# Optimization experiments

Measured on AMD Instinct MI355X. Metric: run time of the kernel, lower is better.

Reference implementation:

```python
import jax, jax.numpy as jnp
import numpy as np
from jax import lax

DN = ('NHWC', 'HWIO', 'NHWC')


def setup_inputs() -> dict:
    key = jax.random.key(0)
    k1, k2, k3, k4, k5, k6 = jax.random.split(key, 6)
    B = 1024
    vals = jax.random.normal(k1, (B, 64, 64, 1), dtype=jnp.float32)
    active = (jax.random.uniform(k2, (B, 64, 64, 1)) < 0.1).astype(jnp.float32)
    x = vals * active
    W1 = jax.random.normal(k3, (3, 3, 1, 64), dtype=jnp.float32) * 0.1
    b1 = jax.random.normal(k4, (64,), dtype=jnp.float32) * 0.1
    W2 = jax.random.normal(k5, (3, 3, 64, 32), dtype=jnp.float32) * 0.05
    b2 = jax.random.normal(k6, (32,), dtype=jnp.float32) * 0.05
    return {"x": x, "W1": W1, "b1": b1, "W2": W2, "b2": b2}


def reference(x, W1, b1, W2, b2):
    # x: [B, 64, 64, 1] NHWC (spconv from_dense layout); active sites = nonzero pixels
    m0 = (jnp.abs(x).max(axis=-1, keepdims=True) > 0).astype(x.dtype)  # [B,64,64,1]
    # SparseConv2d(1,64,3,stride=1, pad=0): output indices = any active input in 3x3 window
    m1 = lax.reduce_window(m0, jnp.array(0, x.dtype), lax.max,
                           (1, 3, 3, 1), (1, 1, 1, 1), 'VALID')  # [B,62,62,1]
    y = lax.conv_general_dilated(x, W1, (1, 1), 'VALID', dimension_numbers=DN)
    y = (y + b1) * m1  # bias only at active output sites; [B,62,62,64]
    # SparseInverseConv2d(64,32,3): transposed conv restricted to the ORIGINAL
    # active index set (indice_key='cp0'), i.e. output only where m0 is active.
    z = lax.conv_transpose(y, W2, (1, 1), 'VALID', dimension_numbers=DN)  # [B,64,64,32]
    z = (z + b2) * m0
    # SparseConvTensor.dense() returns NCHW
    return jnp.transpose(z, (0, 3, 1, 2))
```

## Files before the change

### kernel.cpp

```cpp
#include <hip/hip_runtime.h>

#define BDIM 256
#define KC_STRIDE 28
#define CASE_STRIDE (32 * KC_STRIDE)
#define SP 2052

typedef float floatx4 __attribute__((ext_vector_type(4)));

__device__ __forceinline__ int casef(int p) {
  return ((unsigned)(p - 2) < 60u) ? 2 : (p < 2 ? p : p - 59);
}

__global__ __launch_bounds__(BDIM) void prep_kernel(
    const float* __restrict__ W1, const float* __restrict__ b1,
    const float* __restrict__ W2, const float* __restrict__ b2,
    float* __restrict__ ws) {
  __shared__ float Mlds[9 * 9 * 32];
  __shared__ float BvL[9 * 32];
  const int tid = threadIdx.x;
  const int co = tid & 31;
  for (int tap = tid >> 5; tap < 9; tap += 8) {
    float acc[9] = {0.f, 0.f, 0.f, 0.f, 0.f, 0.f, 0.f, 0.f, 0.f};
    float accB = 0.f;
    for (int ci = 0; ci < 64; ++ci) {
      float w2 = W2[(tap * 64 + ci) * 32 + co];
      accB = fmaf(b1[ci], w2, accB);
#pragma unroll
      for (int e = 0; e < 9; ++e) acc[e] = fmaf(W1[e * 64 + ci], w2, acc[e]);
    }
#pragma unroll
    for (int e = 0; e < 9; ++e) Mlds[(tap * 9 + e) * 32 + co] = acc[e];
    BvL[tap * 32 + co] = accB;
  }
  __syncthreads();

  const int a = blockIdx.x / 5, c = blockIdx.x % 5;
  const int dmask[5] = {4, 6, 7, 3, 1};
  const int Da = dmask[a], Dc = dmask[c];
  for (int t = tid; t < CASE_STRIDE; t += BDIM) {
    int cc = t / KC_STRIDE, r = t % KC_STRIDE;
    float s = 0.f;
    if (r < 25) {
      int u = r / 5, v = r % 5;
      for (int di = 0; di < 3; ++di) {
        if (!((Da >> di) & 1)) continue;
        int ei = u - di;
        if ((unsigned)ei > 2u) continue;
        for (int dj = 0; dj < 3; ++dj) {
          if (!((Dc >> dj) & 1)) continue;
          int ej = v - dj;
          if ((unsigned)ej > 2u) continue;
          s += Mlds[((di * 3 + dj) * 9 + ei * 3 + ej) * 32 + cc];
        }
      }
    } else if (r == 25) {
      s = b2[cc];
      for (int di = 0; di < 3; ++di)
        if ((Da >> di) & 1)
          for (int dj = 0; dj < 3; ++dj)
            if ((Dc >> dj) & 1) s += BvL[(di * 3 + dj) * 32 + cc];
    }
    ws[blockIdx.x * CASE_STRIDE + t] = s;
  }
}

__global__ __launch_bounds__(BDIM) void main_kernel(
    const float* __restrict__ x, const float* __restrict__ ws,
    float* __restrict__ out) {
  const int bb = blockIdx.x;
  const int b = bb >> 1;
  const int r0 = (bb & 1) << 5;
  const int tid = threadIdx.x;
  const int lane = tid & 63;
  const int wave = tid >> 6;

  __shared__ __align__(16) float xp[36 * 68];
  __shared__ __align__(16) float S[8][SP];
  __shared__ __align__(16) float KiL[CASE_STRIDE];
  __shared__ unsigned long long Rm[32];
  __shared__ unsigned short aqi[448], aqb[128];
  __shared__ int nqi_sh, nqb_sh;

  if (tid == 0) { nqi_sh = 0; nqb_sh = 0; }
  float4* xp4 = reinterpret_cast<float4*>(xp);
  for (int i = tid; i < 612; i += BDIM) xp4[i] = make_float4(0.f, 0.f, 0.f, 0.f);
  for (int i = tid; i < CASE_STRIDE; i += BDIM) KiL[i] = ws[12 * CASE_STRIDE + i];
  __syncthreads();

  const float* xb = x + (size_t)b * 4096;
  for (int it = tid; it < 576; it += BDIM) {
    int i = it >> 4, c4 = (it & 15) << 2;
    int r = r0 - 2 + i;
    if ((unsigned)r < 64u) {
      float4 v = *reinterpret_cast<const float4*>(xb + r * 64 + c4);
      float2* d2 = reinterpret_cast<float2*>(&xp[i * 68 + 2 + c4]);
      d2[0] = make_float2(v.x, v.y);
      d2[1] = make_float2(v.z, v.w);
    }
  }
  __syncthreads();

  for (int k = wave; k < 32; k += 4) {
    int pred = (xp[(k + 2) * 68 + 2 + lane] != 0.0f);
    unsigned long long m = __ballot(pred);
    if (lane == 0) Rm[k] = m;
  }
  __syncthreads();

  for (int g = tid; g < 512; g += BDIM) {
    int k = g >> 4, q0 = (g & 15) << 2;
    unsigned bits = (unsigned)(Rm[k] >> q0) & 0xFu;
    if (!bits) continue;
    int p = r0 + k;
    bool inter = ((unsigned)(p - 2) < 60u) && ((unsigned)(q0 - 4) <= 52u);
    if (inter) {
      aqi[atomicAdd(&nqi_sh, 1)] = (unsigned short)g;
    } else {
      aqb[atomicAdd(&nqb_sh, 1)] = (unsigned short)g;
    }
  }
  __syncthreads();

  const int nqi = nqi_sh, nqb = nqb_sh;
  float* outb = out + (size_t)b * (32 * 4096);
  const int co4 = tid & 3;

  for (int cg = 0; cg < 4; ++cg) {
    const int co_lo = (cg << 3) + co4;
    float KA[26], KB[26];
    {
      const float* KpA = &KiL[co_lo * KC_STRIDE];
      const float* KpB = &KiL[(co_lo + 4) * KC_STRIDE];
#pragma unroll
      for (int j = 0; j < 26; ++j) { KA[j] = KpA[j]; KB[j] = KpB[j]; }
    }
    for (int n = tid; n < nqi * 4; n += BDIM) {
      int g = aqi[n >> 2];
      int k = g >> 4, q0 = (g & 15) << 2;
      float ba = KA[25], bbv = KB[25];
      float a0 = ba, a1 = ba, a2 = ba, a3 = ba;
      float b0 = bbv, b1 = bbv, b2 = bbv, b3 = bbv;
#pragma unroll
      for (int u = 0; u < 5; ++u) {
        const float* xr = &xp[(k + u) * 68 + q0];
        float4 xa = *reinterpret_cast<const float4*>(xr);
        float4 xc = *reinterpret_cast<const float4*>(xr + 4);
        float xv[8] = {xa.x, xa.y, xa.z, xa.w, xc.x, xc.y, xc.z, xc.w};
#pragma unroll
        for (int v = 0; v < 5; ++v) {
          float ka = KA[u * 5 + v], kb = KB[u * 5 + v];
          a0 = fmaf(xv[v], ka, a0);
          a1 = fmaf(xv[v + 1], ka, a1);
          a2 = fmaf(xv[v + 2], ka, a2);
          a3 = fmaf(xv[v + 3], ka, a3);
          b0 = fmaf(xv[v], kb, b0);
          b1 = fmaf(xv[v + 1], kb, b1);
          b2 = fmaf(xv[v + 2], kb, b2);
          b3 = fmaf(xv[v + 3], kb, b3);
        }
      }
      int so = (k << 6) + q0;
      *reinterpret_cast<float4*>(&S[co4][so]) = make_float4(a0, a1, a2, a3);
      *reinterpret_cast<float4*>(&S[co4 + 4][so]) = make_float4(b0, b1, b2, b3);
    }
    for (int n = tid; n < nqb * 8; n += BDIM) {
      int g = aqb[n >> 3];
      int cs = n & 7;
      int co = (cg << 3) + cs;
      int k = g >> 4, q0 = (g & 15) << 2;
      int p = r0 + k;
      int cp = casef(p);
      const float* K0 = ws + ((cp * 5 + casef(q0)) * 32 + co) * KC_STRIDE;
      const float* K1 = ws + ((cp * 5 + casef(q0 + 1)) * 32 + co) * KC_STRIDE;
      const float* K2 = ws + ((cp * 5 + casef(q0 + 2)) * 32 + co) * KC_STRIDE;
      const float* K3 = ws + ((cp * 5 + casef(q0 + 3)) * 32 + co) * KC_STRIDE;
      float z0 = K0[25], z1 = K1[25], z2 = K2[25], z3 = K3[25];
#pragma unroll
      for (int u = 0; u < 5; ++u) {
        const float* xr = &xp[(k + u) * 68 + q0];
        float4 xa = *reinterpret_cast<const float4*>(xr);
        float4 xc = *reinterpret_cast<const float4*>(xr + 4);
        float xv[8] = {xa.x, xa.y, xa.z, xa.w, xc.x, xc.y, xc.z, xc.w};
#pragma unroll
        for (int v = 0; v < 5; ++v) {
          int o = u * 5 + v;
          z0 = fmaf(xv[v], K0[o], z0);
          z1 = fmaf(xv[v + 1], K1[o], z1);
          z2 = fmaf(xv[v + 2], K2[o], z2);
          z3 = fmaf(xv[v + 3], K3[o], z3);
        }
      }
      *reinterpret_cast<float4*>(&S[cs][(k << 6) + q0]) =
          make_float4(z0, z1, z2, z3);
    }
    asm volatile("s_waitcnt lgkmcnt(0)" ::: "memory");
    __builtin_amdgcn_s_barrier();
    {
      int co_a = (cg << 3) + wave;
      float* dstA = outb + (((size_t)co_a) << 12) + (r0 << 6);
      float* dstB = outb + (((size_t)(co_a + 4)) << 12) + (r0 << 6);
      const floatx4* SpA = reinterpret_cast<const floatx4*>(&S[wave][0]);
      const floatx4* SpB = reinterpret_cast<const floatx4*>(&S[wave + 4][0]);
#pragma unroll
      for (int i = 0; i < 8; ++i) {
        int f4 = (i << 6) + lane;
        int kk = f4 >> 4, q0 = (f4 & 15) << 2;
        unsigned bits = (unsigned)(Rm[kk] >> q0) & 0xFu;
        floatx4 va = SpA[f4];
        floatx4 vb = SpB[f4];
        if (!(bits & 1u)) { va.x = 0.f; vb.x = 0.f; }
        if (!(bits & 2u)) { va.y = 0.f; vb.y = 0.f; }
        if (!(bits & 4u)) { va.z = 0.f; vb.z = 0.f; }
        if (!(bits & 8u)) { va.w = 0.f; vb.w = 0.f; }
        __builtin_nontemporal_store(va, reinterpret_cast<floatx4*>(dstA + (f4 << 2)));
        __builtin_nontemporal_store(vb, reinterpret_cast<floatx4*>(dstB + (f4 << 2)));
      }
    }
    asm volatile("s_waitcnt lgkmcnt(0)" ::: "memory");
    __builtin_amdgcn_s_barrier();
  }
}

extern "C" void kernel_launch(void* const* d_in, const int* in_sizes, int n_in,
                              void* d_out, int out_size, void* d_ws, size_t ws_size,
                              hipStream_t stream) {
  const float* x  = (const float*)d_in[0];
  const float* W1 = (const float*)d_in[1];
  const float* b1 = (const float*)d_in[2];
  const float* W2 = (const float*)d_in[3];
  const float* b2 = (const float*)d_in[4];
  float* out = (float*)d_out;
  float* ws  = (float*)d_ws;
  int B = in_sizes[0] / 4096;

  hipLaunchKernelGGL(prep_kernel, dim3(25), dim3(BDIM), 0, stream, W1, b1, W2, b2, ws);
  hipLaunchKernelGGL(main_kernel, dim3(2 * B), dim3(BDIM), 0, stream, x, ws, out);
}
```

Baseline: 123.8 us.

## Process whole 64-row image per block instead of half-image blocks

Each block now handles a full 64x64 image instead of a 32-row half, halving the grid to B blocks and removing the two-row halo reloaded by each half. Shared buffers (padded input, staging S, active-group queues) are doubled. This cuts redundant halo loads and per-block setup such as the weight copy into LDS, at the cost of much larger LDS use per block, which lowers occupancy, and fewer blocks to spread across CUs.

```diff
diff --git a/kernel.cpp b/kernel.cpp
--- a/kernel.cpp
+++ b/kernel.cpp
@@ -3,7 +3,7 @@
 #define BDIM 256
 #define KC_STRIDE 28
 #define CASE_STRIDE (32 * KC_STRIDE)
-#define SP 2052
+#define SP 4100
 
 typedef float floatx4 __attribute__((ext_vector_type(4)));
 
@@ -67,51 +67,45 @@
 __global__ __launch_bounds__(BDIM) void main_kernel(
     const float* __restrict__ x, const float* __restrict__ ws,
     float* __restrict__ out) {
-  const int bb = blockIdx.x;
-  const int b = bb >> 1;
-  const int r0 = (bb & 1) << 5;
+  const int b = blockIdx.x;
   const int tid = threadIdx.x;
   const int lane = tid & 63;
   const int wave = tid >> 6;
 
-  __shared__ __align__(16) float xp[36 * 68];
+  __shared__ __align__(16) float xp[68 * 68];
   __shared__ __align__(16) float S[8][SP];
   __shared__ __align__(16) float KiL[CASE_STRIDE];
-  __shared__ unsigned long long Rm[32];
-  __shared__ unsigned short aqi[448], aqb[128];
+  __shared__ unsigned long long Rm[64];
+  __shared__ unsigned short aqi[840], aqb[184];
   __shared__ int nqi_sh, nqb_sh;
 
   if (tid == 0) { nqi_sh = 0; nqb_sh = 0; }
   float4* xp4 = reinterpret_cast<float4*>(xp);
-  for (int i = tid; i < 612; i += BDIM) xp4[i] = make_float4(0.f, 0.f, 0.f, 0.f);
+  for (int i = tid; i < 68 * 68 / 4; i += BDIM) xp4[i] = make_float4(0.f, 0.f, 0.f, 0.f);
   for (int i = tid; i < CASE_STRIDE; i += BDIM) KiL[i] = ws[12 * CASE_STRIDE + i];
   __syncthreads();
 
   const float* xb = x + (size_t)b * 4096;
-  for (int it = tid; it < 576; it += BDIM) {
-    int i = it >> 4, c4 = (it & 15) << 2;
-    int r = r0 - 2 + i;
-    if ((unsigned)r < 64u) {
-      float4 v = *reinterpret_cast<const float4*>(xb + r * 64 + c4);
-      float2* d2 = reinterpret_cast<float2*>(&xp[i * 68 + 2 + c4]);
-      d2[0] = make_float2(v.x, v.y);
-      d2[1] = make_float2(v.z, v.w);
-    }
-  }
-  __syncthreads();
-
-  for (int k = wave; k < 32; k += 4) {
-    int pred = (xp[(k + 2) * 68 + 2 + lane] != 0.0f);
+  for (int it = tid; it < 1024; it += BDIM) {
+    int r = it >> 4, c4 = (it & 15) << 2;
+    float4 v = *reinterpret_cast<const float4*>(xb + r * 64 + c4);
+    float2* d2 = reinterpret_cast<float2*>(&xp[(2 + r) * 68 + 2 + c4]);
+    d2[0] = make_float2(v.x, v.y);
+    d2[1] = make_float2(v.z, v.w);
+  }
+  __syncthreads();
+
+  for (int r = wave; r < 64; r += 4) {
+    int pred = (xp[(2 + r) * 68 + 2 + lane] != 0.0f);
     unsigned long long m = __ballot(pred);
-    if (lane == 0) Rm[k] = m;
-  }
-  __syncthreads();
-
-  for (int g = tid; g < 512; g += BDIM) {
-    int k = g >> 4, q0 = (g & 15) << 2;
-    unsigned bits = (unsigned)(Rm[k] >> q0) & 0xFu;
+    if (lane == 0) Rm[r] = m;
+  }
+  __syncthreads();
+
+  for (int g = tid; g < 1024; g += BDIM) {
+    int p = g >> 4, q0 = (g & 15) << 2;
+    unsigned bits = (unsigned)(Rm[p] >> q0) & 0xFu;
     if (!bits) continue;
-    int p = r0 + k;
     bool inter = ((unsigned)(p - 2) < 60u) && ((unsigned)(q0 - 4) <= 52u);
     if (inter) {
       aqi[atomicAdd(&nqi_sh, 1)] = (unsigned short)g;
@@ -168,8 +162,7 @@
       int cs = n & 7;
       int co = (cg << 3) + cs;
       int k = g >> 4, q0 = (g & 15) << 2;
-      int p = r0 + k;
-      int cp = casef(p);
+      int cp = casef(k);
       const float* K0 = ws + ((cp * 5 + casef(q0)) * 32 + co) * KC_STRIDE;
       const float* K1 = ws + ((cp * 5 + casef(q0 + 1)) * 32 + co) * KC_STRIDE;
       const float* K2 = ws + ((cp * 5 + casef(q0 + 2)) * 32 + co) * KC_STRIDE;
@@ -197,12 +190,12 @@
     __builtin_amdgcn_s_barrier();
     {
       int co_a = (cg << 3) + wave;
-      float* dstA = outb + (((size_t)co_a) << 12) + (r0 << 6);
-      float* dstB = outb + (((size_t)(co_a + 4)) << 12) + (r0 << 6);
+      float* dstA = outb + (((size_t)co_a) << 12);
+      float* dstB = outb + (((size_t)(co_a + 4)) << 12);
       const floatx4* SpA = reinterpret_cast<const floatx4*>(&S[wave][0]);
       const floatx4* SpB = reinterpret_cast<const floatx4*>(&S[wave + 4][0]);
 #pragma unroll
-      for (int i = 0; i < 8; ++i) {
+      for (int i = 0; i < 16; ++i) {
         int f4 = (i << 6) + lane;
         int kk = f4 >> 4, q0 = (f4 & 15) << 2;
         unsigned bits = (unsigned)(Rm[kk] >> q0) & 0xFu;
@@ -234,5 +227,5 @@
   int B = in_sizes[0] / 4096;
 
   hipLaunchKernelGGL(prep_kernel, dim3(25), dim3(BDIM), 0, stream, W1, b1, W2, b2, ws);
-  hipLaunchKernelGGL(main_kernel, dim3(2 * B), dim3(BDIM), 0, stream, x, ws, out);
-}
+  hipLaunchKernelGGL(main_kernel, dim3(B), dim3(BDIM), 0, stream, x, ws, out);
+}
```

New measurement: 147.6 us. 19.2% more time.
